# Performance work log

Measured on AMD Instinct MI355X. Metric: run time of the kernel, lower is better.

Reference implementation:

```python
import jax, jax.numpy as jnp
import numpy as np

C = 1.0          # Poincare ball curvature
NORM_FACTOR = 1.0
EPS = 1e-7
MAX_NORM = (1.0 - 1e-5) / np.sqrt(C)


def _artanh(x):
    x = jnp.clip(x, -1.0 + EPS, 1.0 - EPS)
    return jnp.arctanh(x)


def logmap0(x):
    # tangent vector at origin of Poincare ball (c=C)
    n = jnp.clip(jnp.linalg.norm(x, axis=-1, keepdims=True), EPS, None)
    sc = np.sqrt(C)
    return _artanh(sc * n) * x / (sc * n)


def expmap0(u):
    n = jnp.clip(jnp.linalg.norm(u, axis=-1, keepdims=True), EPS, None)
    sc = np.sqrt(C)
    return jnp.tanh(sc * n) * u / (sc * n)


def proj(x):
    # clip points to stay strictly inside the ball
    n = jnp.clip(jnp.linalg.norm(x, axis=-1, keepdims=True), EPS, None)
    return jnp.where(n > MAX_NORM, x / n * MAX_NORM, x)


def setup_inputs() -> dict:
    key = jax.random.key(0)
    ks = jax.random.split(key, 10)
    B, N, D_IN, D_H, D_LAT, L = 32, 1024, 128, 128, 64, 2
    s_in = 1.0 / np.sqrt(D_IN)
    s_h = 1.0 / np.sqrt(D_H)
    return {
        "node_features": jax.random.normal(ks[0], (B, N, D_IN), jnp.float32),
        "adjacency_matrix": jax.random.uniform(ks[1], (B, N, N), jnp.float32),
        "node_mask": jnp.ones((B, N, 1), jnp.float32),
        "W_embed": jax.random.normal(ks[2], (D_H, D_IN), jnp.float32) * s_in,
        "W_msg": jax.random.normal(ks[3], (L, D_H, D_H), jnp.float32) * s_h,
        "b_msg": jnp.zeros((L, D_H), jnp.float32),
        "W_agg": jax.random.normal(ks[4], (L, D_H, D_H), jnp.float32) * s_h,
        "b_agg": jnp.zeros((L, D_H), jnp.float32),
        "W_proj": jax.random.normal(ks[5], (2 * D_LAT, D_H), jnp.float32) * s_h,
        "b_proj": jnp.zeros((2 * D_LAT,), jnp.float32),
    }


def reference(node_features, adjacency_matrix, node_mask,
              W_embed, W_msg, b_msg, W_agg, b_agg, W_proj, b_proj):
    # feature embedding (bias-free linear, weights live on the manifold);
    # map to the Poincare ball
    h = jnp.einsum('bnd,hd->bnh', node_features, W_embed)
    x = proj(expmap0(h))

    num_layers = W_msg.shape[0]
    for l in range(num_layers):  # small fixed layer count
        t = logmap0(x)                                   # [B,N,D]
        m = t @ W_msg[l] + b_msg[l]                      # message transform
        agg = jnp.einsum('bij,bjd->bid', adjacency_matrix, m) / NORM_FACTOR
        agg = agg @ W_agg[l] + b_agg[l]                  # aggregation transform
        t = jax.nn.relu(m + agg)                         # tangent-space activation
        x = proj(expmap0(t))

    tangent = logmap0(x)                                 # final logmap0 in encode()
    mean_logvar = tangent @ W_proj.T + b_proj            # [B,N,2*latent]
    return mean_logvar * node_mask
```

## Files before the change

### kernel.cpp

```cpp
#include <hip/hip_runtime.h>
#include <hip/hip_bf16.h>

typedef __bf16 bf16;
typedef __bf16 bf16x8 __attribute__((ext_vector_type(8)));
typedef float  floatx4 __attribute__((ext_vector_type(4)));

#define EPSF      1e-7f
#define MAXNORM   0.99999f

__device__ __forceinline__ float sane(float x) {
    return (fabsf(x) < 1e30f) ? x : 0.0f;
}

__device__ __forceinline__ float hyp_scale(float ss) {
    float n  = sqrtf(ss);
    float nh = fmaxf(n, EPSF);
    float s1 = tanhf(nh) / nh;
    float nx = s1 * n;
    if (nx > MAXNORM) { s1 *= MAXNORM / nx; nx = MAXNORM; }
    float nx2 = fmaxf(nx, EPSF);
    return (atanhf(nx2) / nx2) * s1;
}

__device__ __forceinline__ bf16x8 cvt8(float4 a, float4 b) {
    bf16x8 r;
    r[0] = (bf16)a.x; r[1] = (bf16)a.y; r[2] = (bf16)a.z; r[3] = (bf16)a.w;
    r[4] = (bf16)b.x; r[5] = (bf16)b.y; r[6] = (bf16)b.z; r[7] = (bf16)b.w;
    return r;
}

__device__ __forceinline__ int sw128(int row, int k) {
    return row * 128 + (((k >> 3) ^ (row & 15)) << 3) + (k & 7);
}
__device__ __forceinline__ int sw64(int row, int k) {
    return row * 64 + (((k >> 3) ^ (row & 7)) << 3) + (k & 7);
}

template <int MODE>
__global__ __launch_bounds__(256) void gemm128(
    const void* __restrict__ Xv, const float* __restrict__ W,
    const float* __restrict__ bias, const bf16* __restrict__ MaddB,
    const float* __restrict__ MaddF,
    bf16* __restrict__ Y, bf16* __restrict__ YT, float* __restrict__ Yf)
{
    __shared__ __align__(16) bf16 Xs[128 * 128];
    __shared__ __align__(16) bf16 Ws[128 * 128];
    const int tid = threadIdx.x;
    const int bx  = blockIdx.x;

    if (MODE == 0) {
        const float4* Xg = reinterpret_cast<const float4*>(
            (const float*)Xv + (size_t)bx * 16384);
        #pragma unroll
        for (int i = 0; i < 8; ++i) {
            int g = tid + i * 256;
            int row = g >> 4, gc = g & 15;
            float4 v0 = Xg[2 * g], v1 = Xg[2 * g + 1];
            *reinterpret_cast<bf16x8*>(&Xs[row * 128 + ((gc ^ (row & 15)) << 3)]) = cvt8(v0, v1);
        }
    } else {
        const bf16x8* Xg = reinterpret_cast<const bf16x8*>(
            (const bf16*)Xv + (size_t)bx * 16384);
        #pragma unroll
        for (int i = 0; i < 8; ++i) {
            int g = tid + i * 256;
            int row = g >> 4, gc = g & 15;
            bf16x8 v = Xg[g];
            *reinterpret_cast<bf16x8*>(&Xs[row * 128 + ((gc ^ (row & 15)) << 3)]) = v;
        }
    }
    if (MODE == 1 || MODE == 2) {
        const int c0 = (tid & 15) * 8;
        #pragma unroll
        for (int rr = 0; rr < 8; ++rr) {
            int r = (tid >> 4) * 8 + rr;
            const float4* p = reinterpret_cast<const float4*>(W + r * 128 + c0);
            float4 v0 = p[0], v1 = p[1];
            float vv[8] = {v0.x, v0.y, v0.z, v0.w, v1.x, v1.y, v1.z, v1.w};
            #pragma unroll
            for (int j = 0; j < 8; ++j) {
                int n = c0 + j;
                Ws[n * 128 + (((r >> 3) ^ (n & 15)) << 3) + (r & 7)] = (bf16)vv[j];
            }
        }
    } else {
        const float4* Wg = reinterpret_cast<const float4*>(W);
        #pragma unroll
        for (int i = 0; i < 8; ++i) {
            int g = tid + i * 256;
            int row = g >> 4, gc = g & 15;
            float4 v0 = Wg[2 * g], v1 = Wg[2 * g + 1];
            *reinterpret_cast<bf16x8*>(&Ws[row * 128 + ((gc ^ (row & 15)) << 3)]) = cvt8(v0, v1);
        }
    }
    __syncthreads();

    const int lane = tid & 63;
    const int wv   = tid >> 6;
    const int n16  = lane & 15;
    const int quad = lane >> 4;
    const int rbase = wv * 32;

    floatx4 acc[2][8];
    #pragma unroll
    for (int a = 0; a < 2; ++a)
        #pragma unroll
        for (int b = 0; b < 8; ++b) acc[a][b] = (floatx4){0.f, 0.f, 0.f, 0.f};

    #pragma unroll
    for (int kc = 0; kc < 4; ++kc) {
        int k0 = kc * 32 + quad * 8;
        bf16x8 a0 = *reinterpret_cast<const bf16x8*>(&Xs[sw128(rbase + n16, k0)]);
        bf16x8 a1 = *reinterpret_cast<const bf16x8*>(&Xs[sw128(rbase + 16 + n16, k0)]);
        #pragma unroll
        for (int ct = 0; ct < 8; ++ct) {
            bf16x8 b = *reinterpret_cast<const bf16x8*>(&Ws[sw128(ct * 16 + n16, k0)]);
            acc[0][ct] = __builtin_amdgcn_mfma_f32_16x16x32_bf16(a0, b, acc[0][ct], 0, 0, 0);
            acc[1][ct] = __builtin_amdgcn_mfma_f32_16x16x32_bf16(a1, b, acc[1][ct], 0, 0, 0);
        }
    }

    float bv[8];
    #pragma unroll
    for (int ct = 0; ct < 8; ++ct)
        bv[ct] = (MODE != 0) ? sane(bias[ct * 16 + n16]) : 0.0f;

    #pragma unroll
    for (int rt = 0; rt < 2; ++rt) {
        #pragma unroll
        for (int r = 0; r < 4; ++r) {
            const int lrow = rbase + rt * 16 + quad * 4 + r;
            const size_t grow = (size_t)bx * 128 + lrow;
            float u[8];
            #pragma unroll
            for (int ct = 0; ct < 8; ++ct) {
                u[ct] = acc[rt][ct][r] + bv[ct];
                if (MODE == 2)
                    u[ct] = fmaxf(u[ct] + (float)MaddB[grow * 128 + ct * 16 + n16], 0.0f);
                u[ct] = sane(u[ct]);
            }
            if (MODE == 0 || MODE == 2) {
                float ss = 0.f;
                #pragma unroll
                for (int ct = 0; ct < 8; ++ct) ss += u[ct] * u[ct];
                #pragma unroll
                for (int off = 1; off < 16; off <<= 1) ss += __shfl_xor(ss, off);
                float sc = hyp_scale(sane(ss));
                #pragma unroll
                for (int ct = 0; ct < 8; ++ct) u[ct] *= sc;
            }
            if (MODE == 3) {
                float mk = sane(MaddF[grow]);
                #pragma unroll
                for (int ct = 0; ct < 8; ++ct)
                    Yf[grow * 128 + ct * 16 + n16] = sane(u[ct] * mk);
            } else {
                #pragma unroll
                for (int ct = 0; ct < 8; ++ct) {
                    bf16 o = (bf16)sane(u[ct]);
                    Y[grow * 128 + ct * 16 + n16] = o;
                    if (MODE == 1) {
                        size_t bb = grow >> 10, node = grow & 1023;
                        YT[((bb << 7) + ct * 16 + n16) * 1024 + node] = o;
                    }
                }
            }
        }
    }
}

__global__ __launch_bounds__(256) void adjmm(
    const float* __restrict__ Adj, const bf16* __restrict__ mT,
    bf16* __restrict__ agg0)
{
    __shared__ __align__(16) bf16 As[128 * 64];
    __shared__ __align__(16) bf16 Bs[128 * 64];
    const int tid = threadIdx.x;
    const int b   = blockIdx.x >> 3;
    const int mt  = blockIdx.x & 7;
    const float* Ag = Adj + ((size_t)b << 20) + ((size_t)mt << 17);
    const bf16*  Bg = mT  + ((size_t)b << 17);

    const int lane = tid & 63, wv = tid >> 6;
    const int n16 = lane & 15, quad = lane >> 4;
    const int wr = (wv >> 1) * 64, wc = (wv & 1) * 64;

    floatx4 acc[4][4];
    #pragma unroll
    for (int a = 0; a < 4; ++a)
        #pragma unroll
        for (int c = 0; c < 4; ++c) acc[a][c] = (floatx4){0.f, 0.f, 0.f, 0.f};

    for (int kk = 0; kk < 16; ++kk) {
        const int k0 = kk * 64;
        #pragma unroll
        for (int i = 0; i < 4; ++i) {
            int g = tid + i * 256;
            int row = g >> 3, gc = g & 7;
            const float4* pa = reinterpret_cast<const float4*>(
                Ag + (size_t)row * 1024 + k0 + gc * 8);
            float4 a0 = pa[0], a1 = pa[1];
            *reinterpret_cast<bf16x8*>(&As[row * 64 + ((gc ^ (row & 7)) << 3)]) = cvt8(a0, a1);
            bf16x8 vb = *reinterpret_cast<const bf16x8*>(Bg + (size_t)row * 1024 + k0 + gc * 8);
            *reinterpret_cast<bf16x8*>(&Bs[row * 64 + ((gc ^ (row & 7)) << 3)]) = vb;
        }
        __syncthreads();
        #pragma unroll
        for (int kc = 0; kc < 2; ++kc) {
            const int ko = kc * 32 + quad * 8;
            bf16x8 a[4], bb[4];
            #pragma unroll
            for (int rt = 0; rt < 4; ++rt)
                a[rt] = *reinterpret_cast<const bf16x8*>(&As[sw64(wr + rt * 16 + n16, ko)]);
            #pragma unroll
            for (int ct = 0; ct < 4; ++ct)
                bb[ct] = *reinterpret_cast<const bf16x8*>(&Bs[sw64(wc + ct * 16 + n16, ko)]);
            #pragma unroll
            for (int rt = 0; rt < 4; ++rt)
                #pragma unroll
                for (int ct = 0; ct < 4; ++ct)
                    acc[rt][ct] = __builtin_amdgcn_mfma_f32_16x16x32_bf16(a[rt], bb[ct], acc[rt][ct], 0, 0, 0);
        }
        __syncthreads();
    }

    const size_t outBase = ((size_t)b * 1024 + (size_t)mt * 128) * 128;
    #pragma unroll
    for (int rt = 0; rt < 4; ++rt) {
        #pragma unroll
        for (int r = 0; r < 4; ++r) {
            int lrow = wr + rt * 16 + quad * 4 + r;
            #pragma unroll
            for (int ct = 0; ct < 4; ++ct)
                agg0[outBase + (size_t)lrow * 128 + wc + ct * 16 + n16] = (bf16)sane(acc[rt][ct][r]);
        }
    }
}

extern "C" void kernel_launch(void* const* d_in, const int* in_sizes, int n_in,
                              void* d_out, int out_size, void* d_ws, size_t ws_size,
                              hipStream_t stream)
{
    const float* X    = (const float*)d_in[0];
    const float* Adj  = (const float*)d_in[1];
    const float* Mask = (const float*)d_in[2];
    const float* Wemb = (const float*)d_in[3];
    const float* Wmsg = (const float*)d_in[4];
    const float* bmsg = (const float*)d_in[5];
    const float* Wagg = (const float*)d_in[6];
    const float* bagg = (const float*)d_in[7];
    const float* Wprj = (const float*)d_in[8];
    const float* bprj = (const float*)d_in[9];
    float* out = (float*)d_out;

    const size_t BN = 32768;
    bf16* buf0 = (bf16*)d_ws;
    bf16* buf1 = buf0 + BN * 128;
    bf16* buf2 = buf1 + BN * 128;

    dim3 grid(256), blk(256);

    gemm128<0><<<grid, blk, 0, stream>>>(X, Wemb, nullptr, nullptr, nullptr,
                                         buf0, nullptr, nullptr);
    gemm128<1><<<grid, blk, 0, stream>>>(buf0, Wmsg, bmsg, nullptr, nullptr,
                                         buf1, buf2, nullptr);
    adjmm<<<grid, blk, 0, stream>>>(Adj, buf2, buf0);
    gemm128<2><<<grid, blk, 0, stream>>>(buf0, Wagg, bagg, buf1, nullptr,
                                         buf2, nullptr, nullptr);
    gemm128<1><<<grid, blk, 0, stream>>>(buf2, Wmsg + 16384, bmsg + 128, nullptr, nullptr,
                                         buf1, buf0, nullptr);
    adjmm<<<grid, blk, 0, stream>>>(Adj, buf0, buf2);
    gemm128<2><<<grid, blk, 0, stream>>>(buf2, Wagg + 16384, bagg + 128, buf1, nullptr,
                                         buf0, nullptr, nullptr);
    gemm128<3><<<grid, blk, 0, stream>>>(buf0, Wprj, bprj, nullptr, Mask,
                                         nullptr, nullptr, out);
}
```

Baseline: 362.6 us.

## Fuse GCN pipeline into three kernels with double-buffered adjacency GEMM

Collapses the eight-kernel sequence into three. One kernel does embedding plus message transform, and two fused adjacency kernels each chain the adjacency GEMM, aggregation transform, relu/hyperbolic rescale and the next message or projection GEMM through shared memory. The adjacency GEMM moves to 512 threads with register-staged double buffering, block order is remapped so the tiles of one batch are spread across blocks, and the `sane` clamps are removed. This cuts kernel launches and intermediate global round-trips at the cost of heavier shared memory use, which may lower occupancy.

```diff
diff --git a/kernel.cpp b/kernel.cpp
--- a/kernel.cpp
+++ b/kernel.cpp
@@ -5,12 +5,9 @@
 typedef __bf16 bf16x8 __attribute__((ext_vector_type(8)));
 typedef float  floatx4 __attribute__((ext_vector_type(4)));
 
-#define EPSF      1e-7f
-#define MAXNORM   0.99999f
-
-__device__ __forceinline__ float sane(float x) {
-    return (fabsf(x) < 1e30f) ? x : 0.0f;
-}
+#define EPSF    1e-7f
+#define MAXNORM 0.99999f
+#define TS_LD   136
 
 __device__ __forceinline__ float hyp_scale(float ss) {
     float n  = sqrtf(ss);
@@ -36,77 +33,60 @@
     return row * 64 + (((k >> 3) ^ (row & 7)) << 3) + (k & 7);
 }
 
-template <int MODE>
-__global__ __launch_bounds__(256) void gemm128(
-    const void* __restrict__ Xv, const float* __restrict__ W,
-    const float* __restrict__ bias, const bf16* __restrict__ MaddB,
-    const float* __restrict__ MaddF,
-    bf16* __restrict__ Y, bf16* __restrict__ YT, float* __restrict__ Yf)
+__global__ __launch_bounds__(256) void embed_msg(
+    const float* __restrict__ X, const float* __restrict__ Wemb,
+    const float* __restrict__ Wmsg, const float* __restrict__ bmsg,
+    bf16* __restrict__ M, bf16* __restrict__ MT)
 {
     __shared__ __align__(16) bf16 Xs[128 * 128];
     __shared__ __align__(16) bf16 Ws[128 * 128];
-    const int tid = threadIdx.x;
-    const int bx  = blockIdx.x;
-
-    if (MODE == 0) {
-        const float4* Xg = reinterpret_cast<const float4*>(
-            (const float*)Xv + (size_t)bx * 16384);
+    __shared__ __align__(16) bf16 W2[128 * 128];
+    __shared__ __align__(16) bf16 Ts[128 * TS_LD];
+    const int tid = threadIdx.x, bx = blockIdx.x;
+
+    {
+        const float4* Xg = reinterpret_cast<const float4*>(X + (size_t)bx * 16384);
         #pragma unroll
         for (int i = 0; i < 8; ++i) {
-            int g = tid + i * 256;
-            int row = g >> 4, gc = g & 15;
+            int g = tid + i * 256, row = g >> 4, gc = g & 15;
             float4 v0 = Xg[2 * g], v1 = Xg[2 * g + 1];
             *reinterpret_cast<bf16x8*>(&Xs[row * 128 + ((gc ^ (row & 15)) << 3)]) = cvt8(v0, v1);
         }
-    } else {
-        const bf16x8* Xg = reinterpret_cast<const bf16x8*>(
-            (const bf16*)Xv + (size_t)bx * 16384);
+    }
+    {
+        const float4* Wg = reinterpret_cast<const float4*>(Wemb);
         #pragma unroll
         for (int i = 0; i < 8; ++i) {
-            int g = tid + i * 256;
-            int row = g >> 4, gc = g & 15;
-            bf16x8 v = Xg[g];
-            *reinterpret_cast<bf16x8*>(&Xs[row * 128 + ((gc ^ (row & 15)) << 3)]) = v;
-        }
-    }
-    if (MODE == 1 || MODE == 2) {
+            int g = tid + i * 256, row = g >> 4, gc = g & 15;
+            float4 v0 = Wg[2 * g], v1 = Wg[2 * g + 1];
+            *reinterpret_cast<bf16x8*>(&Ws[row * 128 + ((gc ^ (row & 15)) << 3)]) = cvt8(v0, v1);
+        }
+    }
+    {
         const int c0 = (tid & 15) * 8;
         #pragma unroll
         for (int rr = 0; rr < 8; ++rr) {
             int r = (tid >> 4) * 8 + rr;
-            const float4* p = reinterpret_cast<const float4*>(W + r * 128 + c0);
+            const float4* p = reinterpret_cast<const float4*>(Wmsg + r * 128 + c0);
             float4 v0 = p[0], v1 = p[1];
             float vv[8] = {v0.x, v0.y, v0.z, v0.w, v1.x, v1.y, v1.z, v1.w};
             #pragma unroll
             for (int j = 0; j < 8; ++j) {
                 int n = c0 + j;
-                Ws[n * 128 + (((r >> 3) ^ (n & 15)) << 3) + (r & 7)] = (bf16)vv[j];
-            }
-        }
-    } else {
-        const float4* Wg = reinterpret_cast<const float4*>(W);
-        #pragma unroll
-        for (int i = 0; i < 8; ++i) {
-            int g = tid + i * 256;
-            int row = g >> 4, gc = g & 15;
-            float4 v0 = Wg[2 * g], v1 = Wg[2 * g + 1];
-            *reinterpret_cast<bf16x8*>(&Ws[row * 128 + ((gc ^ (row & 15)) << 3)]) = cvt8(v0, v1);
+                W2[n * 128 + (((r >> 3) ^ (n & 15)) << 3) + (r & 7)] = (bf16)vv[j];
+            }
         }
     }
     __syncthreads();
 
-    const int lane = tid & 63;
-    const int wv   = tid >> 6;
-    const int n16  = lane & 15;
-    const int quad = lane >> 4;
+    const int lane = tid & 63, wv = tid >> 6, n16 = lane & 15, quad = lane >> 4;
     const int rbase = wv * 32;
 
     floatx4 acc[2][8];
     #pragma unroll
     for (int a = 0; a < 2; ++a)
         #pragma unroll
-        for (int b = 0; b < 8; ++b) acc[a][b] = (floatx4){0.f, 0.f, 0.f, 0.f};
-
+        for (int c = 0; c < 8; ++c) acc[a][c] = (floatx4){0.f, 0.f, 0.f, 0.f};
     #pragma unroll
     for (int kc = 0; kc < 4; ++kc) {
         int k0 = kc * 32 + quad * 8;
@@ -119,120 +99,261 @@
             acc[1][ct] = __builtin_amdgcn_mfma_f32_16x16x32_bf16(a1, b, acc[1][ct], 0, 0, 0);
         }
     }
-
+    #pragma unroll
+    for (int rt = 0; rt < 2; ++rt) {
+        #pragma unroll
+        for (int r = 0; r < 4; ++r) {
+            int row = rbase + rt * 16 + quad * 4 + r;
+            float u[8], ss = 0.f;
+            #pragma unroll
+            for (int ct = 0; ct < 8; ++ct) { u[ct] = acc[rt][ct][r]; ss += u[ct] * u[ct]; }
+            #pragma unroll
+            for (int off = 1; off < 16; off <<= 1) ss += __shfl_xor(ss, off);
+            float sc = hyp_scale(ss);
+            #pragma unroll
+            for (int ct = 0; ct < 8; ++ct)
+                Ts[row * TS_LD + ct * 16 + n16] = (bf16)(u[ct] * sc);
+        }
+    }
+    __syncthreads();
+
+    floatx4 acc2[2][8];
+    #pragma unroll
+    for (int a = 0; a < 2; ++a)
+        #pragma unroll
+        for (int c = 0; c < 8; ++c) acc2[a][c] = (floatx4){0.f, 0.f, 0.f, 0.f};
+    #pragma unroll
+    for (int kc = 0; kc < 4; ++kc) {
+        int k0 = kc * 32 + quad * 8;
+        bf16x8 a0 = *reinterpret_cast<const bf16x8*>(&Ts[(rbase + n16) * TS_LD + k0]);
+        bf16x8 a1 = *reinterpret_cast<const bf16x8*>(&Ts[(rbase + 16 + n16) * TS_LD + k0]);
+        #pragma unroll
+        for (int ct = 0; ct < 8; ++ct) {
+            bf16x8 b = *reinterpret_cast<const bf16x8*>(&W2[sw128(ct * 16 + n16, k0)]);
+            acc2[0][ct] = __builtin_amdgcn_mfma_f32_16x16x32_bf16(a0, b, acc2[0][ct], 0, 0, 0);
+            acc2[1][ct] = __builtin_amdgcn_mfma_f32_16x16x32_bf16(a1, b, acc2[1][ct], 0, 0, 0);
+        }
+    }
     float bv[8];
     #pragma unroll
-    for (int ct = 0; ct < 8; ++ct)
-        bv[ct] = (MODE != 0) ? sane(bias[ct * 16 + n16]) : 0.0f;
-
+    for (int ct = 0; ct < 8; ++ct) bv[ct] = bmsg[ct * 16 + n16];
     #pragma unroll
     for (int rt = 0; rt < 2; ++rt) {
         #pragma unroll
         for (int r = 0; r < 4; ++r) {
-            const int lrow = rbase + rt * 16 + quad * 4 + r;
-            const size_t grow = (size_t)bx * 128 + lrow;
-            float u[8];
+            int lrow = rbase + rt * 16 + quad * 4 + r;
+            size_t grow = (size_t)bx * 128 + lrow;
             #pragma unroll
             for (int ct = 0; ct < 8; ++ct) {
-                u[ct] = acc[rt][ct][r] + bv[ct];
-                if (MODE == 2)
-                    u[ct] = fmaxf(u[ct] + (float)MaddB[grow * 128 + ct * 16 + n16], 0.0f);
-                u[ct] = sane(u[ct]);
-            }
-            if (MODE == 0 || MODE == 2) {
-                float ss = 0.f;
-                #pragma unroll
-                for (int ct = 0; ct < 8; ++ct) ss += u[ct] * u[ct];
-                #pragma unroll
-                for (int off = 1; off < 16; off <<= 1) ss += __shfl_xor(ss, off);
-                float sc = hyp_scale(sane(ss));
-                #pragma unroll
-                for (int ct = 0; ct < 8; ++ct) u[ct] *= sc;
-            }
-            if (MODE == 3) {
-                float mk = sane(MaddF[grow]);
-                #pragma unroll
-                for (int ct = 0; ct < 8; ++ct)
-                    Yf[grow * 128 + ct * 16 + n16] = sane(u[ct] * mk);
-            } else {
-                #pragma unroll
-                for (int ct = 0; ct < 8; ++ct) {
-                    bf16 o = (bf16)sane(u[ct]);
-                    Y[grow * 128 + ct * 16 + n16] = o;
-                    if (MODE == 1) {
-                        size_t bb = grow >> 10, node = grow & 1023;
-                        YT[((bb << 7) + ct * 16 + n16) * 1024 + node] = o;
-                    }
-                }
-            }
-        }
-    }
-}
-
-__global__ __launch_bounds__(256) void adjmm(
-    const float* __restrict__ Adj, const bf16* __restrict__ mT,
-    bf16* __restrict__ agg0)
+                bf16 o = (bf16)(acc2[rt][ct][r] + bv[ct]);
+                M[grow * 128 + ct * 16 + n16] = o;
+                MT[((grow >> 10) * 128 + ct * 16 + n16) * 1024 + (grow & 1023)] = o;
+            }
+        }
+    }
+}
+
+template <int LAST>
+__global__ __launch_bounds__(512) void adj_fused(
+    const float* __restrict__ Adj, const bf16* __restrict__ MT,
+    const bf16* __restrict__ Mprev,
+    const float* __restrict__ Wagg, const float* __restrict__ bagg,
+    const float* __restrict__ W2f,  const float* __restrict__ b2,
+    const float* __restrict__ Mask,
+    bf16* __restrict__ Mout, bf16* __restrict__ MTout, float* __restrict__ Out)
 {
-    __shared__ __align__(16) bf16 As[128 * 64];
-    __shared__ __align__(16) bf16 Bs[128 * 64];
-    const int tid = threadIdx.x;
-    const int b   = blockIdx.x >> 3;
-    const int mt  = blockIdx.x & 7;
+    __shared__ __align__(16) bf16 smem[4 * 128 * 64];
+    __shared__ __align__(16) bf16 Ts[128 * TS_LD];
+    bf16* As0 = smem;
+    bf16* As1 = smem + 128 * 64;
+    bf16* Bs0 = smem + 2 * 128 * 64;
+    bf16* Bs1 = smem + 3 * 128 * 64;
+
+    const int tid = threadIdx.x, bid = blockIdx.x;
+    const int mt = bid >> 5, b = bid & 31;
     const float* Ag = Adj + ((size_t)b << 20) + ((size_t)mt << 17);
-    const bf16*  Bg = mT  + ((size_t)b << 17);
-
-    const int lane = tid & 63, wv = tid >> 6;
-    const int n16 = lane & 15, quad = lane >> 4;
-    const int wr = (wv >> 1) * 64, wc = (wv & 1) * 64;
-
-    floatx4 acc[4][4];
+    const bf16*  Bg = MT  + ((size_t)b << 17);
+
+    const int lane = tid & 63, wv = tid >> 6, n16 = lane & 15, quad = lane >> 4;
+    const int wr = (wv >> 2) * 64, wc = (wv & 3) * 32;
+
+    floatx4 acc[4][2];
     #pragma unroll
     for (int a = 0; a < 4; ++a)
         #pragma unroll
-        for (int c = 0; c < 4; ++c) acc[a][c] = (floatx4){0.f, 0.f, 0.f, 0.f};
-
+        for (int c = 0; c < 2; ++c) acc[a][c] = (floatx4){0.f, 0.f, 0.f, 0.f};
+
+    float4 pa[2][2]; bf16x8 pb[2];
+    auto load_regs = [&](int kk) {
+        #pragma unroll
+        for (int i = 0; i < 2; ++i) {
+            int g = tid + i * 512, row = g >> 3, gc = g & 7;
+            const float4* pA = reinterpret_cast<const float4*>(
+                Ag + (size_t)row * 1024 + kk * 64 + gc * 8);
+            pa[i][0] = pA[0]; pa[i][1] = pA[1];
+            pb[i] = *reinterpret_cast<const bf16x8*>(Bg + (size_t)row * 1024 + kk * 64 + gc * 8);
+        }
+    };
+    auto store_lds = [&](bf16* A, bf16* B) {
+        #pragma unroll
+        for (int i = 0; i < 2; ++i) {
+            int g = tid + i * 512, row = g >> 3, gc = g & 7;
+            *reinterpret_cast<bf16x8*>(&A[row * 64 + ((gc ^ (row & 7)) << 3)]) = cvt8(pa[i][0], pa[i][1]);
+            *reinterpret_cast<bf16x8*>(&B[row * 64 + ((gc ^ (row & 7)) << 3)]) = pb[i];
+        }
+    };
+
+    load_regs(0);
+    store_lds(As0, Bs0);
     for (int kk = 0; kk < 16; ++kk) {
-        const int k0 = kk * 64;
-        #pragma unroll
-        for (int i = 0; i < 4; ++i) {
-            int g = tid + i * 256;
-            int row = g >> 3, gc = g & 7;
-            const float4* pa = reinterpret_cast<const float4*>(
-                Ag + (size_t)row * 1024 + k0 + gc * 8);
-            float4 a0 = pa[0], a1 = pa[1];
-            *reinterpret_cast<bf16x8*>(&As[row * 64 + ((gc ^ (row & 7)) << 3)]) = cvt8(a0, a1);
-            bf16x8 vb = *reinterpret_cast<const bf16x8*>(Bg + (size_t)row * 1024 + k0 + gc * 8);
-            *reinterpret_cast<bf16x8*>(&Bs[row * 64 + ((gc ^ (row & 7)) << 3)]) = vb;
-        }
+        bf16* Acur = (kk & 1) ? As1 : As0;
+        bf16* Bcur = (kk & 1) ? Bs1 : Bs0;
+        bf16* Anxt = (kk & 1) ? As0 : As1;
+        bf16* Bnxt = (kk & 1) ? Bs0 : Bs1;
+        if (kk < 15) load_regs(kk + 1);
         __syncthreads();
         #pragma unroll
         for (int kc = 0; kc < 2; ++kc) {
-            const int ko = kc * 32 + quad * 8;
-            bf16x8 a[4], bb[4];
+            int ko = kc * 32 + quad * 8;
+            bf16x8 a[4], bb[2];
             #pragma unroll
             for (int rt = 0; rt < 4; ++rt)
-                a[rt] = *reinterpret_cast<const bf16x8*>(&As[sw64(wr + rt * 16 + n16, ko)]);
-            #pragma unroll
-            for (int ct = 0; ct < 4; ++ct)
-                bb[ct] = *reinterpret_cast<const bf16x8*>(&Bs[sw64(wc + ct * 16 + n16, ko)]);
+                a[rt] = *reinterpret_cast<const bf16x8*>(&Acur[sw64(wr + rt * 16 + n16, ko)]);
+            #pragma unroll
+            for (int ct = 0; ct < 2; ++ct)
+                bb[ct] = *reinterpret_cast<const bf16x8*>(&Bcur[sw64(wc + ct * 16 + n16, ko)]);
             #pragma unroll
             for (int rt = 0; rt < 4; ++rt)
                 #pragma unroll
-                for (int ct = 0; ct < 4; ++ct)
+                for (int ct = 0; ct < 2; ++ct)
                     acc[rt][ct] = __builtin_amdgcn_mfma_f32_16x16x32_bf16(a[rt], bb[ct], acc[rt][ct], 0, 0, 0);
         }
-        __syncthreads();
-    }
-
-    const size_t outBase = ((size_t)b * 1024 + (size_t)mt * 128) * 128;
-    #pragma unroll
-    for (int rt = 0; rt < 4; ++rt) {
+        if (kk < 15) store_lds(Anxt, Bnxt);
+    }
+    __syncthreads();
+
+    #pragma unroll
+    for (int rt = 0; rt < 4; ++rt)
+        #pragma unroll
+        for (int ct = 0; ct < 2; ++ct)
+            #pragma unroll
+            for (int r = 0; r < 4; ++r) {
+                int row = wr + rt * 16 + quad * 4 + r, col = wc + ct * 16 + n16;
+                Ts[row * TS_LD + col] = (bf16)acc[rt][ct][r];
+            }
+
+    bf16* Wa = smem;
+    bf16* W2 = smem + 128 * 128;
+    {
+        const int c0 = (tid & 15) * 8;
+        #pragma unroll
+        for (int rr = 0; rr < 4; ++rr) {
+            int r = (tid >> 4) * 4 + rr;
+            const float4* p = reinterpret_cast<const float4*>(Wagg + r * 128 + c0);
+            float4 v0 = p[0], v1 = p[1];
+            float vv[8] = {v0.x, v0.y, v0.z, v0.w, v1.x, v1.y, v1.z, v1.w};
+            #pragma unroll
+            for (int j = 0; j < 8; ++j) {
+                int n = c0 + j;
+                Wa[n * 128 + (((r >> 3) ^ (n & 15)) << 3) + (r & 7)] = (bf16)vv[j];
+            }
+        }
+    }
+    if (LAST) {
+        const float4* Wg = reinterpret_cast<const float4*>(W2f);
+        #pragma unroll
+        for (int i = 0; i < 4; ++i) {
+            int g = tid + i * 512, row = g >> 4, gc = g & 15;
+            float4 v0 = Wg[2 * g], v1 = Wg[2 * g + 1];
+            *reinterpret_cast<bf16x8*>(&W2[row * 128 + ((gc ^ (row & 15)) << 3)]) = cvt8(v0, v1);
+        }
+    } else {
+        const int c0 = (tid & 15) * 8;
+        #pragma unroll
+        for (int rr = 0; rr < 4; ++rr) {
+            int r = (tid >> 4) * 4 + rr;
+            const float4* p = reinterpret_cast<const float4*>(W2f + r * 128 + c0);
+            float4 v0 = p[0], v1 = p[1];
+            float vv[8] = {v0.x, v0.y, v0.z, v0.w, v1.x, v1.y, v1.z, v1.w};
+            #pragma unroll
+            for (int j = 0; j < 8; ++j) {
+                int n = c0 + j;
+                W2[n * 128 + (((r >> 3) ^ (n & 15)) << 3) + (r & 7)] = (bf16)vv[j];
+            }
+        }
+    }
+    __syncthreads();
+
+    const int rbase = wv * 16;
+    const size_t growbase = (size_t)b * 1024 + (size_t)mt * 128;
+    floatx4 acc2[8];
+    #pragma unroll
+    for (int c = 0; c < 8; ++c) acc2[c] = (floatx4){0.f, 0.f, 0.f, 0.f};
+    #pragma unroll
+    for (int kc = 0; kc < 4; ++kc) {
+        int k0 = kc * 32 + quad * 8;
+        bf16x8 a = *reinterpret_cast<const bf16x8*>(&Ts[(rbase + n16) * TS_LD + k0]);
+        #pragma unroll
+        for (int ct = 0; ct < 8; ++ct) {
+            bf16x8 bb = *reinterpret_cast<const bf16x8*>(&Wa[sw128(ct * 16 + n16, k0)]);
+            acc2[ct] = __builtin_amdgcn_mfma_f32_16x16x32_bf16(a, bb, acc2[ct], 0, 0, 0);
+        }
+    }
+    {
+        float bva[8];
+        #pragma unroll
+        for (int ct = 0; ct < 8; ++ct) bva[ct] = bagg[ct * 16 + n16];
         #pragma unroll
         for (int r = 0; r < 4; ++r) {
-            int lrow = wr + rt * 16 + quad * 4 + r;
-            #pragma unroll
-            for (int ct = 0; ct < 4; ++ct)
-                agg0[outBase + (size_t)lrow * 128 + wc + ct * 16 + n16] = (bf16)sane(acc[rt][ct][r]);
+            int row = rbase + quad * 4 + r;
+            size_t grow = growbase + row;
+            float u[8], ss = 0.f;
+            #pragma unroll
+            for (int ct = 0; ct < 8; ++ct) {
+                u[ct] = fmaxf(acc2[ct][r] + bva[ct] + (float)Mprev[grow * 128 + ct * 16 + n16], 0.f);
+                ss += u[ct] * u[ct];
+            }
+            #pragma unroll
+            for (int off = 1; off < 16; off <<= 1) ss += __shfl_xor(ss, off);
+            float sc = hyp_scale(ss);
+            #pragma unroll
+            for (int ct = 0; ct < 8; ++ct)
+                Ts[row * TS_LD + ct * 16 + n16] = (bf16)(u[ct] * sc);
+        }
+    }
+
+    floatx4 acc3[8];
+    #pragma unroll
+    for (int c = 0; c < 8; ++c) acc3[c] = (floatx4){0.f, 0.f, 0.f, 0.f};
+    #pragma unroll
+    for (int kc = 0; kc < 4; ++kc) {
+        int k0 = kc * 32 + quad * 8;
+        bf16x8 a = *reinterpret_cast<const bf16x8*>(&Ts[(rbase + n16) * TS_LD + k0]);
+        #pragma unroll
+        for (int ct = 0; ct < 8; ++ct) {
+            bf16x8 bb = *reinterpret_cast<const bf16x8*>(&W2[sw128(ct * 16 + n16, k0)]);
+            acc3[ct] = __builtin_amdgcn_mfma_f32_16x16x32_bf16(a, bb, acc3[ct], 0, 0, 0);
+        }
+    }
+    float bv2[8];
+    #pragma unroll
+    for (int ct = 0; ct < 8; ++ct) bv2[ct] = b2[ct * 16 + n16];
+    #pragma unroll
+    for (int r = 0; r < 4; ++r) {
+        int row = rbase + quad * 4 + r;
+        size_t grow = growbase + row;
+        if (LAST) {
+            float mk = Mask[grow];
+            #pragma unroll
+            for (int ct = 0; ct < 8; ++ct)
+                Out[grow * 128 + ct * 16 + n16] = (acc3[ct][r] + bv2[ct]) * mk;
+        } else {
+            #pragma unroll
+            for (int ct = 0; ct < 8; ++ct) {
+                bf16 o = (bf16)(acc3[ct][r] + bv2[ct]);
+                Mout[grow * 128 + ct * 16 + n16] = o;
+                MTout[((grow >> 10) * 128 + ct * 16 + n16) * 1024 + (grow & 1023)] = o;
+            }
         }
     }
 }
@@ -254,24 +375,16 @@
     float* out = (float*)d_out;
 
     const size_t BN = 32768;
-    bf16* buf0 = (bf16*)d_ws;
-    bf16* buf1 = buf0 + BN * 128;
-    bf16* buf2 = buf1 + BN * 128;
-
-    dim3 grid(256), blk(256);
-
-    gemm128<0><<<grid, blk, 0, stream>>>(X, Wemb, nullptr, nullptr, nullptr,
-                                         buf0, nullptr, nullptr);
-    gemm128<1><<<grid, blk, 0, stream>>>(buf0, Wmsg, bmsg, nullptr, nullptr,
-                                         buf1, buf2, nullptr);
-    adjmm<<<grid, blk, 0, stream>>>(Adj, buf2, buf0);
-    gemm128<2><<<grid, blk, 0, stream>>>(buf0, Wagg, bagg, buf1, nullptr,
-                                         buf2, nullptr, nullptr);
-    gemm128<1><<<grid, blk, 0, stream>>>(buf2, Wmsg + 16384, bmsg + 128, nullptr, nullptr,
-                                         buf1, buf0, nullptr);
-    adjmm<<<grid, blk, 0, stream>>>(Adj, buf0, buf2);
-    gemm128<2><<<grid, blk, 0, stream>>>(buf2, Wagg + 16384, bagg + 128, buf1, nullptr,
-                                         buf0, nullptr, nullptr);
-    gemm128<3><<<grid, blk, 0, stream>>>(buf0, Wprj, bprj, nullptr, Mask,
-                                         nullptr, nullptr, out);
-}
+    bf16* m0  = (bf16*)d_ws;
+    bf16* m0T = m0  + BN * 128;
+    bf16* m1  = m0T + BN * 128;
+    bf16* m1T = m1  + BN * 128;
+
+    embed_msg<<<256, 256, 0, stream>>>(X, Wemb, Wmsg, bmsg, m0, m0T);
+    adj_fused<0><<<256, 512, 0, stream>>>(Adj, m0T, m0, Wagg, bagg,
+                                          Wmsg + 16384, bmsg + 128, nullptr,
+                                          m1, m1T, nullptr);
+    adj_fused<1><<<256, 512, 0, stream>>>(Adj, m1T, m1, Wagg + 16384, bagg + 128,
+                                          Wprj, bprj, Mask,
+                                          nullptr, nullptr, out);
+}
```

Result: faster. 304.0 us (-16.2%).
